# Performance work log

Hardware: AMD Instinct MI355X
Metric: run time of the kernel (lower is better)

## Reference

```python
import jax, jax.numpy as jnp
import numpy as np

B, L, C = 256, 256, 128
HID, H = 128, 4
D = HID // H            # 32
NUM_LAYERS = 2
NEG_SLOPE = 0.2
LN_EPS = 1e-5


def setup_inputs() -> dict:
    key = jax.random.key(0)
    ks = jax.random.split(key, 16)
    E = 4096
    x = jax.random.normal(ks[0], (B, L, C), dtype=jnp.float32)
    edge_index = jax.random.randint(ks[1], (2, E), 0, C, dtype=jnp.int64)
    s_in = 1.0 / np.sqrt(L)
    s_h = 1.0 / np.sqrt(HID)
    return {
        "x": x,
        "edge_index": edge_index,
        "emb_W": jax.random.normal(ks[2], (L, HID), jnp.float32) * s_in,
        "emb_b": jnp.zeros((HID,), jnp.float32),
        "lin_l_W": jax.random.normal(ks[3], (NUM_LAYERS, HID, HID), jnp.float32) * s_h,
        "lin_l_b": jnp.zeros((NUM_LAYERS, HID), jnp.float32),
        "lin_r_W": jax.random.normal(ks[4], (NUM_LAYERS, HID, HID), jnp.float32) * s_h,
        "lin_r_b": jnp.zeros((NUM_LAYERS, HID), jnp.float32),
        "att": jax.random.normal(ks[5], (NUM_LAYERS, H, D), jnp.float32) * (1.0 / np.sqrt(D)),
        "gat_bias": jnp.zeros((NUM_LAYERS, HID), jnp.float32),
        "ln_gamma": jnp.ones((NUM_LAYERS, HID), jnp.float32),
        "ln_beta": jnp.zeros((NUM_LAYERS, HID), jnp.float32),
        "proj_W": jax.random.normal(ks[6], (HID, L), jnp.float32) * s_h,
        "proj_b": jnp.zeros((L,), jnp.float32),
    }


def _batch_edges(edge_index):
    # replicate single-graph edges per batch sample with node offsets, then add self loops
    E = edge_index.shape[1]
    off = jnp.repeat(jnp.arange(B, dtype=edge_index.dtype) * C, E)
    src = jnp.tile(edge_index[0], B) + off
    dst = jnp.tile(edge_index[1], B) + off
    loop = jnp.arange(B * C, dtype=edge_index.dtype)
    return jnp.concatenate([src, loop]), jnp.concatenate([dst, loop])


def _layer_norm(x, g, b):
    mu = jnp.mean(x, axis=-1, keepdims=True)
    var = jnp.mean(jnp.square(x - mu), axis=-1, keepdims=True)
    return (x - mu) * jax.lax.rsqrt(var + LN_EPS) * g + b


def _gatv2(x, src, dst, Wl, bl, Wr, br, a, bias):
    N = x.shape[0]
    xl = (x @ Wl + bl).reshape(N, H, D)   # source-side transform
    xr = (x @ Wr + br).reshape(N, H, D)   # target-side transform
    e = jax.nn.leaky_relu(xl[src] + xr[dst], NEG_SLOPE)   # (E', H, D)
    logits = jnp.einsum('ehd,hd->eh', e, a)               # (E', H)
    m = jax.ops.segment_max(logits, dst, num_segments=N)
    p = jnp.exp(logits - m[dst])
    s = jax.ops.segment_sum(p, dst, num_segments=N)
    alpha = p / (s[dst] + 1e-16)
    out = jax.ops.segment_sum(xl[src] * alpha[:, :, None], dst, num_segments=N)
    return out.reshape(N, HID) + bias, alpha


def reference(x, edge_index, emb_W, emb_b, lin_l_W, lin_l_b, lin_r_W, lin_r_b,
              att, gat_bias, ln_gamma, ln_beta, proj_W, proj_b):
    src, dst = _batch_edges(edge_index)
    # (B, L, C) -> nodes are channels: (B*C, L) -> embed to HID
    h = x.transpose(0, 2, 1).reshape(B * C, L) @ emb_W + emb_b
    alpha = None
    for i in range(NUM_LAYERS):
        new_h, alpha = _gatv2(h, src, dst, lin_l_W[i], lin_l_b[i],
                              lin_r_W[i], lin_r_b[i], att[i], gat_bias[i])
        new_h = jax.nn.elu(new_h)
        h = h + new_h
        h = _layer_norm(h, ln_gamma[i], ln_beta[i])
        # dropout: eval mode, identity
    # attention map (to_dense_adj semantics: adj[b, src%C, dst%C] = mean_h(alpha), then transpose)
    b_idx = src // C
    dense = jnp.zeros((B, C, C), x.dtype).at[b_idx, src % C, dst % C].add(alpha.mean(axis=-1))
    attn_map = dense.transpose(0, 2, 1)
    out = (h @ proj_W + proj_b).reshape(B, C, L).transpose(0, 2, 1)  # (B, L, C)
    return out, attn_map
```

## Files before the change

### kernel.cpp

```cpp
#include <hip/hip_runtime.h>
#include <hip/hip_fp16.h>
#include <math.h>

#define BB 256
#define LL 256
#define CC 128
#define HIDD 128
#define HH 4
#define DD 32
#define EE 4096
#define NN (BB*CC)
#define LN_EPS 1e-5f

typedef short bf16x8 __attribute__((ext_vector_type(8)));
typedef _Float16 f16x8 __attribute__((ext_vector_type(8)));
typedef float f32x4 __attribute__((ext_vector_type(4)));

__device__ __forceinline__ float red64(float p) {
    p += __shfl_xor(p, 32);
    p += __shfl_xor(p, 16);
    p += __shfl_xor(p, 8);
    p += __shfl_xor(p, 4);
    p += __shfl_xor(p, 2);
    p += __shfl_xor(p, 1);
    return p;
}
__device__ __forceinline__ unsigned bfr(float f) {
    unsigned x = __float_as_uint(f);
    return (x + 0x7FFFu + ((x >> 16) & 1u)) >> 16;
}
__device__ __forceinline__ unsigned pack2(float a, float b) { return bfr(a) | (bfr(b) << 16); }
__device__ __forceinline__ float b2f(unsigned u) { return __uint_as_float(u << 16); }
__device__ __forceinline__ __half2 u2h(unsigned u) { __half2 r; *(unsigned*)&r = u; return r; }
__device__ __forceinline__ unsigned h2u(__half2 h) { return *(unsigned*)&h; }

__device__ __forceinline__ void stage_bf16_rm(ushort* lds, const ushort* src, int ldm, int t) {
    #pragma unroll
    for (int i = 0; i < 8; ++i) {
        int flat = i*256 + t;
        int r = flat >> 4, c = flat & 15;
        uint4 pk = *(const uint4*)(src + (size_t)r*ldm + c*8);
        *(uint4*)&lds[((r*16) + (c ^ (r & 7)))*8] = pk;
    }
}
__device__ __forceinline__ void mfma_tile_128(const ushort* Als, const ushort* Bls,
                                              f32x4 acc[2][8], int w, int lane) {
    int mr = lane & 15, quad = lane >> 4;
    #pragma unroll
    for (int ks = 0; ks < 4; ++ks) {
        int ca = ks*4 + quad;
        bf16x8 a[2], b[8];
        #pragma unroll
        for (int mf = 0; mf < 2; ++mf) {
            int m = w*32 + mf*16 + mr;
            a[mf] = *(const bf16x8*)&Als[((m*16) + (ca ^ (m & 7)))*8];
        }
        #pragma unroll
        for (int nf = 0; nf < 8; ++nf) {
            int n = nf*16 + mr;
            b[nf] = *(const bf16x8*)&Bls[((n*16) + (ca ^ (n & 7)))*8];
        }
        #pragma unroll
        for (int mf = 0; mf < 2; ++mf)
            #pragma unroll
            for (int nf = 0; nf < 8; ++nf)
                acc[mf][nf] = __builtin_amdgcn_mfma_f32_16x16x32_bf16(a[mf], b[nf], acc[mf][nf], 0, 0, 0);
    }
}
#define ZERO_ACC(acc) { _Pragma("unroll") for (int i_=0;i_<2;++i_) { _Pragma("unroll") for (int j_=0;j_<8;++j_) acc[i_][j_] = (f32x4){0.f,0.f,0.f,0.f}; } }

__global__ __launch_bounds__(256) void prep_weights(const float* __restrict__ emb_W,
                                                    const float* __restrict__ lWl,
                                                    const float* __restrict__ lWr,
                                                    const float* __restrict__ pW,
                                                    ushort* __restrict__ WembT,
                                                    ushort* __restrict__ WlrT,
                                                    ushort* __restrict__ WpT) {
    int gid = blockIdx.x * 256 + threadIdx.x;
    float v[8];
    if (gid < 4096) {
        int f = gid >> 5, ch = gid & 31;
        #pragma unroll
        for (int j = 0; j < 8; ++j) v[j] = emb_W[(size_t)(ch*8 + j)*HIDD + f];
        uint4 pk; pk.x = pack2(v[0],v[1]); pk.y = pack2(v[2],v[3]);
        pk.z = pack2(v[4],v[5]); pk.w = pack2(v[6],v[7]);
        *(uint4*)&WembT[(size_t)f*LL + ch*8] = pk;
    } else if (gid < 12288) {
        int g = gid - 4096;
        int mat = g >> 11, f = (g >> 4) & 127, ch = g & 15;
        const float* src = ((mat & 1) ? lWr : lWl) + (size_t)(mat >> 1)*HIDD*HIDD;
        #pragma unroll
        for (int j = 0; j < 8; ++j) v[j] = src[(size_t)(ch*8 + j)*HIDD + f];
        uint4 pk; pk.x = pack2(v[0],v[1]); pk.y = pack2(v[2],v[3]);
        pk.z = pack2(v[4],v[5]); pk.w = pack2(v[6],v[7]);
        *(uint4*)&WlrT[(size_t)mat*HIDD*HIDD + (size_t)f*HIDD + ch*8] = pk;
    } else {
        int g = gid - 12288;
        int l = g >> 4, ch = g & 15;
        #pragma unroll
        for (int j = 0; j < 8; ++j) v[j] = pW[(size_t)(ch*8 + j)*LL + l];
        uint4 pk; pk.x = pack2(v[0],v[1]); pk.y = pack2(v[2],v[3]);
        pk.z = pack2(v[4],v[5]); pk.w = pack2(v[6],v[7]);
        *(uint4*)&WpT[(size_t)l*HIDD + ch*8] = pk;
    }
}

__global__ __launch_bounds__(256) void build_lnm(const int* __restrict__ edge,
                                                 __half* __restrict__ lnm_ds) {
    __shared__ int cnt[CC*CC];
    int t = threadIdx.x;
    for (int i = t; i < CC*CC; i += 256) cnt[i] = 0;
    __syncthreads();
    for (int j = t; j < EE; j += 256) {
        int s = edge[j], d = edge[EE + j];
        atomicAdd(&cnt[s*CC + d], 1);
    }
    __syncthreads();
    for (int o = t; o < CC*CC; o += 256) {
        int dstc = o >> 7, srcc = o & 127;
        int c = cnt[srcc*CC + dstc] + ((srcc == dstc) ? 1 : 0);
        lnm_ds[o] = __float2half(c > 0 ? logf((float)c) : -30000.f);
    }
}

__global__ __launch_bounds__(256) void embed_mfma(const float* __restrict__ x,
                                                  const ushort* __restrict__ WembT,
                                                  const float* __restrict__ bias,
                                                  ushort* __restrict__ hout) {
    __shared__ __align__(16) ushort Als[128*16*8];
    __shared__ __align__(16) ushort Bls[128*16*8];
    int b = blockIdx.x;
    int t = threadIdx.x, lane = t & 63, w = t >> 6;
    const float* xb = x + (size_t)b * LL * CC;
    f32x4 acc[2][8];
    ZERO_ACC(acc)
    #pragma unroll
    for (int kh = 0; kh < 2; ++kh) {
        if (kh) __syncthreads();
        #pragma unroll
        for (int i = 0; i < 8; ++i) {
            int flat = i*256 + t;
            int r = flat >> 4, cc = flat & 15;
            float v[8];
            #pragma unroll
            for (int j = 0; j < 8; ++j)
                v[j] = xb[(size_t)(kh*128 + cc*8 + j)*CC + r];
            uint4 pk; pk.x = pack2(v[0],v[1]); pk.y = pack2(v[2],v[3]);
            pk.z = pack2(v[4],v[5]); pk.w = pack2(v[6],v[7]);
            *(uint4*)&Als[((r*16) + (cc ^ (r & 7)))*8] = pk;
        }
        stage_bf16_rm(Bls, WembT + kh*128, LL, t);
        __syncthreads();
        mfma_tile_128(Als, Bls, acc, w, lane);
    }
    int mr = lane & 15, quad = lane >> 4;
    #pragma unroll
    for (int nf = 0; nf < 8; ++nf) {
        int f = nf*16 + mr;
        float bv = bias[f];
        #pragma unroll
        for (int mf = 0; mf < 2; ++mf)
            #pragma unroll
            for (int r = 0; r < 4; ++r) {
                int node = w*32 + mf*16 + quad*4 + r;
                hout[((size_t)b*CC + node)*HIDD + f] = (ushort)bfr(acc[mf][nf][r] + bv);
            }
    }
}

__global__ __launch_bounds__(256) void lin_mfma(const ushort* __restrict__ hmat,
                                                const ushort* __restrict__ WlT,
                                                const ushort* __restrict__ WrT,
                                                const float* __restrict__ bl,
                                                const float* __restrict__ br,
                                                __half* __restrict__ xlT,
                                                __half* __restrict__ xrT) {
    __shared__ __align__(16) ushort Als[128*16*8];
    __shared__ __align__(16) ushort Bls[128*16*8];
    int b = blockIdx.x;
    int t = threadIdx.x, lane = t & 63, w = t >> 6;
    int mr = lane & 15, quad = lane >> 4;
    stage_bf16_rm(Als, hmat + (size_t)b*CC*HIDD, HIDD, t);
    #pragma unroll
    for (int lr = 0; lr < 2; ++lr) {
        if (lr) __syncthreads();
        stage_bf16_rm(Bls, lr ? WrT : WlT, HIDD, t);
        __syncthreads();
        f32x4 acc[2][8];
        ZERO_ACC(acc)
        mfma_tile_128(Als, Bls, acc, w, lane);
        const float* bias = lr ? br : bl;
        __half* out = lr ? xrT : xlT;
        #pragma unroll
        for (int nf = 0; nf < 8; ++nf) {
            int f = nf*16 + mr;
            float bv = bias[f];
            int h = f >> 5, d = f & 31;
            #pragma unroll
            for (int mf = 0; mf < 2; ++mf)
                #pragma unroll
                for (int r = 0; r < 4; ++r) {
                    int node = w*32 + mf*16 + quad*4 + r;
                    out[(((size_t)b*HH + h)*CC + node)*DD + d] = __float2half(acc[mf][nf][r] + bv);
                }
        }
    }
}

__global__ __launch_bounds__(256, 4) void gat_logits(const __half* __restrict__ xl_h,
                                                     const __half* __restrict__ xr_h,
                                                     const __half* __restrict__ lnm_ds,
                                                     const float* __restrict__ att,
                                                     __half* __restrict__ Pg) {
    __shared__ __align__(16) __half xl_lds[CC*DD];
    __shared__ float Slq[CC];
    __shared__ float rpart[2][CC];
    __shared__ float spart[2][CC];

    int bh = blockIdx.x;
    int h = bh & 3;
    int t = threadIdx.x;
    int sg = t >> 7, dst = t & 127;

    {
        const uint4* sp = (const uint4*)(xl_h + (size_t)bh * CC * DD);
        uint4* dp = (uint4*)xl_lds;
        dp[t] = sp[t];
        dp[t + 256] = sp[t + 256];
    }
    __half2 qa2[16], xr2[16];
    const float* ag = att + h*DD;
    #pragma unroll
    for (int c = 0; c < 8; ++c) {
        float4 av = *(const float4*)&ag[c*4];
        qa2[2*c+0] = __floats2half2_rn(0.4f*av.x, 0.4f*av.y);
        qa2[2*c+1] = __floats2half2_rn(0.4f*av.z, 0.4f*av.w);
    }
    float Srq = 0.f;
    {
        uint4 X[4];
        const uint4* xp = (const uint4*)(xr_h + ((size_t)bh*CC + dst)*DD);
        #pragma unroll
        for (int c = 0; c < 4; ++c) X[c] = xp[c];
        const __half2* xv = (const __half2*)X;
        #pragma unroll
        for (int i = 0; i < 16; ++i) {
            xr2[i] = xv[i];
            __half2 p = __hmul2(qa2[i], xr2[i]);
            Srq += __low2float(p) + __high2float(p);
        }
    }
    __syncthreads();

    if (t < CC) {
        uint4 R[4];
        const uint4* rp = (const uint4*)&xl_lds[t*DD];
        #pragma unroll
        for (int c = 0; c < 4; ++c) R[c] = rp[c];
        const __half2* rv = (const __half2*)R;
        __half2 s = __floats2half2_rn(0.f, 0.f);
        #pragma unroll
        for (int i = 0; i < 16; ++i) s = __hfma2(qa2[i], rv[i], s);
        Slq[t] = __low2float(s) + __high2float(s);
    }
    __syncthreads();

    const __half* lrow = lnm_ds + (size_t)dst*CC + sg*64;
    float fSrq = 1.5f * Srq;
    __half2 lv2[32];
    float pmax = -3.0e38f;
    #pragma unroll
    for (int jc = 0; jc < 8; ++jc) {
        int chunk = sg*8 + jc;
        uint4 lu = *(const uint4*)&lrow[jc*8];
        const __half* lnmv = (const __half*)&lu;
        float lf[8];
        #pragma unroll
        for (int e = 0; e < 8; ++e) {
            int src = chunk*8 + e;
            uint4 R[4];
            const uint4* rp = (const uint4*)&xl_lds[src*DD];
            #pragma unroll
            for (int c = 0; c < 4; ++c) R[c] = rp[c];
            const __half2* xv = (const __half2*)R;
            __half2 a0 = __floats2half2_rn(0.f,0.f), a1 = a0, a2 = a0, a3 = a0;
            #pragma unroll
            for (int q = 0; q < 4; ++q) {
                a0 = __hfma2(qa2[4*q+0], __habs2(__hadd2(xv[4*q+0], xr2[4*q+0])), a0);
                a1 = __hfma2(qa2[4*q+1], __habs2(__hadd2(xv[4*q+1], xr2[4*q+1])), a1);
                a2 = __hfma2(qa2[4*q+2], __habs2(__hadd2(xv[4*q+2], xr2[4*q+2])), a2);
                a3 = __hfma2(qa2[4*q+3], __habs2(__hadd2(xv[4*q+3], xr2[4*q+3])), a3);
            }
            __half2 ts = __hadd2(__hadd2(a0, a1), __hadd2(a2, a3));
            float T = __low2float(ts) + __high2float(ts);
            float l = fmaf(1.5f, Slq[src], fSrq + T) + __half2float(lnmv[e]);
            pmax = fmaxf(pmax, l);
            lf[e] = l;
        }
        lv2[jc*4+0] = __floats2half2_rn(lf[0], lf[1]);
        lv2[jc*4+1] = __floats2half2_rn(lf[2], lf[3]);
        lv2[jc*4+2] = __floats2half2_rn(lf[4], lf[5]);
        lv2[jc*4+3] = __floats2half2_rn(lf[6], lf[7]);
    }

    rpart[sg][dst] = pmax;
    __syncthreads();
    float m = fmaxf(rpart[0][dst], rpart[1][dst]);
    float ssum = 0.f;
    #pragma unroll
    for (int i = 0; i < 32; ++i) {
        float e0 = __expf(__low2float(lv2[i]) - m);
        float e1 = __expf(__high2float(lv2[i]) - m);
        ssum += e0 + e1;
        lv2[i] = __floats2half2_rn(e0, e1);
    }
    spart[sg][dst] = ssum;
    __syncthreads();
    float is = 1.f / (spart[0][dst] + spart[1][dst] + 1e-16f);

    __half* pgr = Pg + (size_t)bh*CC*CC + (size_t)dst*CC + sg*64;
    #pragma unroll
    for (int jc = 0; jc < 8; ++jc) {
        __align__(16) __half ov[8];
        #pragma unroll
        for (int i = 0; i < 4; ++i) {
            __half2 v = lv2[jc*4+i];
            ov[2*i+0] = __float2half(__low2float(v) * is);
            ov[2*i+1] = __float2half(__high2float(v) * is);
        }
        *(uint4*)&pgr[jc*8] = *(uint4*)ov;
    }
}

__global__ __launch_bounds__(256) void gat_pv(const __half* __restrict__ Pg,
                                              const __half* __restrict__ xl_h,
                                              __half* __restrict__ xagg) {
    __shared__ __align__(16) __half xl_lds[CC*DD];
    __shared__ __align__(16) __half xlT_swz[DD*16*8];
    int bh = blockIdx.x, h = bh & 3, b = bh >> 2;
    int t = threadIdx.x, lane = t & 63, w = t >> 6;
    {
        const uint4* sp = (const uint4*)(xl_h + (size_t)bh * CC * DD);
        uint4* dp = (uint4*)xl_lds;
        dp[t] = sp[t];
        dp[t + 256] = sp[t + 256];
    }
    __syncthreads();
    for (int i = t; i < 512; i += 256) {
        int f = i >> 4, c = i & 15;
        __align__(16) __half v[8];
        #pragma unroll
        for (int e = 0; e < 8; ++e) v[e] = xl_lds[(c*8 + e)*DD + f];
        *(uint4*)&xlT_swz[((f*16) + (c ^ (f & 7)))*8] = *(uint4*)v;
    }
    __syncthreads();

    int mr = lane & 15, quad = lane >> 4;
    const __half* pb = Pg + (size_t)bh * CC * CC;
    f16x8 a[2][4];
    #pragma unroll
    for (int mf = 0; mf < 2; ++mf) {
        int dr = w*32 + mf*16 + mr;
        #pragma unroll
        for (int ks = 0; ks < 4; ++ks)
            a[mf][ks] = *(const f16x8*)&pb[(size_t)dr*CC + ks*32 + quad*8];
    }
    f32x4 acc[2][2];
    #pragma unroll
    for (int i = 0; i < 2; ++i)
        #pragma unroll
        for (int j = 0; j < 2; ++j) acc[i][j] = (f32x4){0.f,0.f,0.f,0.f};
    #pragma unroll
    for (int ks = 0; ks < 4; ++ks) {
        int ca = ks*4 + quad;
        f16x8 bfrag[2];
        #pragma unroll
        for (int nf = 0; nf < 2; ++nf) {
            int nn = nf*16 + mr;
            bfrag[nf] = *(const f16x8*)&xlT_swz[((nn*16) + (ca ^ (nn & 7)))*8];
        }
        #pragma unroll
        for (int mf = 0; mf < 2; ++mf)
            #pragma unroll
            for (int nf = 0; nf < 2; ++nf)
                acc[mf][nf] = __builtin_amdgcn_mfma_f32_16x16x32_f16(a[mf][ks], bfrag[nf], acc[mf][nf], 0, 0, 0);
    }
    #pragma unroll
    for (int mf = 0; mf < 2; ++mf)
        #pragma unroll
        for (int r = 0; r < 4; ++r) {
            int drow = w*32 + mf*16 + quad*4 + r;
            #pragma unroll
            for (int nf = 0; nf < 2; ++nf) {
                int f = nf*16 + mr;
                xagg[(((size_t)b*CC + drow)*HH + h)*DD + f] = __float2half(acc[mf][nf][r]);
            }
        }
}

__global__ __launch_bounds__(256) void gat_epilogue(const __half* __restrict__ xagg,
                                                    const float* __restrict__ gbias,
                                                    const float* __restrict__ ln_g,
                                                    const float* __restrict__ ln_b,
                                                    const __half* __restrict__ Pws,
                                                    ushort* __restrict__ hmat,
                                                    float* __restrict__ attn_out) {
    __shared__ float wred[4], wred2[4];
    int t = threadIdx.x;
    int nl = t >> 7, f = t & 127;
    int node = blockIdx.x*2 + nl;
    int b = node >> 7, dstc = node & 127;

    float o = __half2float(xagg[(size_t)node*HIDD + f]) + gbias[f];
    o = o > 0.f ? o : (__expf(o) - 1.f);
    float hv = b2f((unsigned)hmat[(size_t)node*HIDD + f]) + o;

    float sum = red64(hv);
    if ((t & 63) == 0) wred[t >> 6] = sum;
    __syncthreads();
    float mean = (wred[nl*2] + wred[nl*2+1]) * 0.0078125f;
    float d = hv - mean;
    float q = red64(d * d);
    if ((t & 63) == 0) wred2[t >> 6] = q;
    __syncthreads();
    float var = (wred2[nl*2] + wred2[nl*2+1]) * 0.0078125f;
    hmat[(size_t)node*HIDD + f] = (ushort)bfr(d * rsqrtf(var + LN_EPS) * ln_g[f] + ln_b[f]);

    if (attn_out) {
        float a = 0.f;
        #pragma unroll
        for (int hh = 0; hh < HH; ++hh)
            a += __half2float(Pws[(((size_t)(b*HH + hh)*CC) + dstc)*CC + f]);
        attn_out[(size_t)node*CC + f] = 0.25f * a;
    }
}

__global__ __launch_bounds__(256) void proj_mfma(const ushort* __restrict__ hmat,
                                                 const ushort* __restrict__ WpT,
                                                 const float* __restrict__ bias,
                                                 float* __restrict__ out) {
    __shared__ __align__(16) ushort Als[128*16*8];
    __shared__ __align__(16) ushort Bls[128*16*8];
    int l0 = blockIdx.x * 128;
    int b  = blockIdx.y;
    int t = threadIdx.x, lane = t & 63, w = t >> 6;
    f32x4 acc[2][8];
    ZERO_ACC(acc)
    stage_bf16_rm(Als, WpT + (size_t)l0*HIDD, HIDD, t);
    stage_bf16_rm(Bls, hmat + (size_t)b*CC*HIDD, HIDD, t);
    __syncthreads();
    mfma_tile_128(Als, Bls, acc, w, lane);
    int mr = lane & 15, quad = lane >> 4;
    #pragma unroll
    for (int nf = 0; nf < 8; ++nf) {
        int c = nf*16 + mr;
        #pragma unroll
        for (int mf = 0; mf < 2; ++mf)
            #pragma unroll
            for (int r = 0; r < 4; ++r) {
                int l = l0 + w*32 + mf*16 + quad*4 + r;
                out[((size_t)b*LL + l)*CC + c] = acc[mf][nf][r] + bias[l];
            }
    }
}

extern "C" void kernel_launch(void* const* d_in, const int* in_sizes, int n_in,
                              void* d_out, int out_size, void* d_ws, size_t ws_size,
                              hipStream_t stream) {
    const float* x        = (const float*)d_in[0];
    const int*   edge     = (const int*)d_in[1];
    const float* emb_W    = (const float*)d_in[2];
    const float* emb_b    = (const float*)d_in[3];
    const float* lin_l_W  = (const float*)d_in[4];
    const float* lin_l_b  = (const float*)d_in[5];
    const float* lin_r_W  = (const float*)d_in[6];
    const float* lin_r_b  = (const float*)d_in[7];
    const float* att      = (const float*)d_in[8];
    const float* gat_bias = (const float*)d_in[9];
    const float* ln_g     = (const float*)d_in[10];
    const float* ln_b     = (const float*)d_in[11];
    const float* proj_W   = (const float*)d_in[12];
    const float* proj_b   = (const float*)d_in[13];

    ushort* h     = (ushort*)d_ws;
    __half* xl_h  = (__half*)(h + (size_t)NN * HIDD);
    __half* xr_h  = xl_h + (size_t)NN * HIDD;
    __half* xagg  = xr_h + (size_t)NN * HIDD;
    __half* Pg    = xagg + (size_t)NN * HIDD;
    __half* lnm_ds = Pg + (size_t)BB * HH * CC * CC;
    ushort* WembT = (ushort*)(lnm_ds + (size_t)CC * CC);
    ushort* WlrT  = WembT + (size_t)CC*LL;
    ushort* WpT   = WlrT + (size_t)4*HIDD*HIDD;

    float* out0 = (float*)d_out;
    float* attn = out0 + (size_t)BB * LL * CC;

    build_lnm<<<1, 256, 0, stream>>>(edge, lnm_ds);
    prep_weights<<<64, 256, 0, stream>>>(emb_W, lin_l_W, lin_r_W, proj_W, WembT, WlrT, WpT);
    embed_mfma<<<BB, 256, 0, stream>>>(x, WembT, emb_b, h);
    for (int layer = 0; layer < 2; ++layer) {
        lin_mfma<<<BB, 256, 0, stream>>>(h,
            WlrT + (size_t)(layer*2 + 0)*HIDD*HIDD,
            WlrT + (size_t)(layer*2 + 1)*HIDD*HIDD,
            lin_l_b + layer*HIDD, lin_r_b + layer*HIDD,
            xl_h, xr_h);
        gat_logits<<<BB*HH, 256, 0, stream>>>(xl_h, xr_h, lnm_ds,
            att + layer*HIDD, Pg);
        gat_pv<<<BB*HH, 256, 0, stream>>>(Pg, xl_h, xagg);
        gat_epilogue<<<NN/2, 256, 0, stream>>>(xagg,
            gat_bias + layer*HIDD, ln_g + layer*HIDD, ln_b + layer*HIDD,
            (layer == 1) ? Pg : nullptr, h, (layer == 1) ? attn : nullptr);
    }
    proj_mfma<<<dim3(2, BB), 256, 0, stream>>>(h, WpT, proj_b, out0);
}
```

Before: 305.9 us.

## Fuse GAT logits/softmax with P·V MFMA and split destinations across blocks

Merges the attention-logit/softmax kernel and the P·xl aggregation kernel into one kernel. The normalized probabilities are kept in LDS in MFMA fragment layout instead of being written to and reread from global memory, and the global P buffer is written only for the last layer, where the attention map needs it. Each block now handles 64 destination nodes with 4 source groups instead of 128 destinations with 2 groups, doubling the grid, and LDS loads of xl rows are double-buffered in registers. The cost is more LDS per block, duplicated xl staging and transposition in both halves, and a fragment-ordered P layout that the epilogue must index to match.

Measured after the change: 296.7 us. 3.0% less time.

```diff
diff --git a/kernel.cpp b/kernel.cpp
--- a/kernel.cpp
+++ b/kernel.cpp
@@ -31,8 +31,6 @@
 }
 __device__ __forceinline__ unsigned pack2(float a, float b) { return bfr(a) | (bfr(b) << 16); }
 __device__ __forceinline__ float b2f(unsigned u) { return __uint_as_float(u << 16); }
-__device__ __forceinline__ __half2 u2h(unsigned u) { __half2 r; *(unsigned*)&r = u; return r; }
-__device__ __forceinline__ unsigned h2u(__half2 h) { return *(unsigned*)&h; }
 
 __device__ __forceinline__ void stage_bf16_rm(ushort* lds, const ushort* src, int ldm, int t) {
     #pragma unroll
@@ -207,20 +205,30 @@
     }
 }
 
-__global__ __launch_bounds__(256, 4) void gat_logits(const __half* __restrict__ xl_h,
-                                                     const __half* __restrict__ xr_h,
-                                                     const __half* __restrict__ lnm_ds,
-                                                     const float* __restrict__ att,
-                                                     __half* __restrict__ Pg) {
+#define LOADC(Rdst, jcv) { _Pragma("unroll") for (int u_ = 0; u_ < 4; ++u_) { \
+    const uint4* rp_ = (const uint4*)&xl_lds[(sg*32 + (jcv)*4 + u_)*DD]; \
+    Rdst[u_][0]=rp_[0]; Rdst[u_][1]=rp_[1]; Rdst[u_][2]=rp_[2]; Rdst[u_][3]=rp_[3]; } }
+
+__global__ __launch_bounds__(256, 4) void gat_fused(const __half* __restrict__ xl_h,
+                                                    const __half* __restrict__ xr_h,
+                                                    const __half* __restrict__ lnm_ds,
+                                                    const float* __restrict__ att,
+                                                    __half* __restrict__ xagg,
+                                                    __half* __restrict__ Pg) {
     __shared__ __align__(16) __half xl_lds[CC*DD];
+    __shared__ __align__(16) __half xlT_swz[DD*16*8];
+    __shared__ __align__(16) __half Pfrag[4*4*64*8];
     __shared__ float Slq[CC];
-    __shared__ float rpart[2][CC];
-    __shared__ float spart[2][CC];
-
-    int bh = blockIdx.x;
-    int h = bh & 3;
+    __shared__ float rpart[4][64];
+    __shared__ float spart[4][64];
+
+    int blk = blockIdx.x;
+    int bh = blk >> 1, dhalf = blk & 1;
+    int h = bh & 3, b = bh >> 2;
     int t = threadIdx.x;
-    int sg = t >> 7, dst = t & 127;
+    int sg = t >> 6, dl = t & 63;
+    int dst = dhalf*64 + dl;
+    int lane = t & 63, w = t >> 6;
 
     {
         const uint4* sp = (const uint4*)(xl_h + (size_t)bh * CC * DD);
@@ -228,6 +236,14 @@
         dp[t] = sp[t];
         dp[t + 256] = sp[t + 256];
     }
+    __align__(16) __half lnm_l[32];
+    {
+        const __half* lrow = lnm_ds + (size_t)dst*CC + sg*32;
+        *(uint4*)&lnm_l[0]  = *(const uint4*)&lrow[0];
+        *(uint4*)&lnm_l[8]  = *(const uint4*)&lrow[8];
+        *(uint4*)&lnm_l[16] = *(const uint4*)&lrow[16];
+        *(uint4*)&lnm_l[24] = *(const uint4*)&lrow[24];
+    }
     __half2 qa2[16], xr2[16];
     const float* ag = att + h*DD;
     #pragma unroll
@@ -261,28 +277,33 @@
         __half2 s = __floats2half2_rn(0.f, 0.f);
         #pragma unroll
         for (int i = 0; i < 16; ++i) s = __hfma2(qa2[i], rv[i], s);
-        Slq[t] = __low2float(s) + __high2float(s);
-    }
-    __syncthreads();
-
-    const __half* lrow = lnm_ds + (size_t)dst*CC + sg*64;
+        Slq[t] = 1.5f * (__low2float(s) + __high2float(s));
+    }
+    for (int i = t; i < 512; i += 256) {
+        int f = i >> 4, c = i & 15;
+        __align__(16) __half v[8];
+        #pragma unroll
+        for (int e = 0; e < 8; ++e) v[e] = xl_lds[(c*8 + e)*DD + f];
+        *(uint4*)&xlT_swz[((f*16) + (c ^ (f & 7)))*8] = *(uint4*)v;
+    }
+    __syncthreads();
+
     float fSrq = 1.5f * Srq;
-    __half2 lv2[32];
-    float pmax = -3.0e38f;
+    __half2 lv2[16];
+    float pm0 = -3.0e38f, pm1 = pm0, pm2 = pm0, pm3 = pm0;
+    uint4 Ra[4][4], Rb[4][4];
+    LOADC(Ra, 0)
+    float lfbuf = 0.f;
     #pragma unroll
     for (int jc = 0; jc < 8; ++jc) {
-        int chunk = sg*8 + jc;
-        uint4 lu = *(const uint4*)&lrow[jc*8];
-        const __half* lnmv = (const __half*)&lu;
-        float lf[8];
-        #pragma unroll
-        for (int e = 0; e < 8; ++e) {
-            int src = chunk*8 + e;
-            uint4 R[4];
-            const uint4* rp = (const uint4*)&xl_lds[src*DD];
-            #pragma unroll
-            for (int c = 0; c < 4; ++c) R[c] = rp[c];
-            const __half2* xv = (const __half2*)R;
+        uint4 (*Rc)[4] = (jc & 1) ? Rb : Ra;
+        uint4 (*Rn)[4] = (jc & 1) ? Ra : Rb;
+        if (jc < 7) LOADC(Rn, jc + 1)
+        #pragma unroll
+        for (int u = 0; u < 4; ++u) {
+            int j = jc*4 + u;
+            int src = sg*32 + j;
+            const __half2* xv = (const __half2*)(Rc[u]);
             __half2 a0 = __floats2half2_rn(0.f,0.f), a1 = a0, a2 = a0, a3 = a0;
             #pragma unroll
             for (int q = 0; q < 4; ++q) {
@@ -293,109 +314,82 @@
             }
             __half2 ts = __hadd2(__hadd2(a0, a1), __hadd2(a2, a3));
             float T = __low2float(ts) + __high2float(ts);
-            float l = fmaf(1.5f, Slq[src], fSrq + T) + __half2float(lnmv[e]);
-            pmax = fmaxf(pmax, l);
-            lf[e] = l;
-        }
-        lv2[jc*4+0] = __floats2half2_rn(lf[0], lf[1]);
-        lv2[jc*4+1] = __floats2half2_rn(lf[2], lf[3]);
-        lv2[jc*4+2] = __floats2half2_rn(lf[4], lf[5]);
-        lv2[jc*4+3] = __floats2half2_rn(lf[6], lf[7]);
-    }
-
-    rpart[sg][dst] = pmax;
-    __syncthreads();
-    float m = fmaxf(rpart[0][dst], rpart[1][dst]);
-    float ssum = 0.f;
-    #pragma unroll
-    for (int i = 0; i < 32; ++i) {
+            float l = (fSrq + T) + Slq[src] + __half2float(lnm_l[j]);
+            if (u == 0)      pm0 = fmaxf(pm0, l);
+            else if (u == 1) pm1 = fmaxf(pm1, l);
+            else if (u == 2) pm2 = fmaxf(pm2, l);
+            else             pm3 = fmaxf(pm3, l);
+            if ((j & 1) == 0) lfbuf = l;
+            else              lv2[j >> 1] = __floats2half2_rn(lfbuf, l);
+        }
+    }
+
+    rpart[sg][dl] = fmaxf(fmaxf(pm0, pm1), fmaxf(pm2, pm3));
+    __syncthreads();
+    float m = fmaxf(fmaxf(rpart[0][dl], rpart[1][dl]),
+                    fmaxf(rpart[2][dl], rpart[3][dl]));
+    float s0 = 0.f, s1 = 0.f, s2 = 0.f, s3 = 0.f;
+    #pragma unroll
+    for (int i = 0; i < 16; ++i) {
         float e0 = __expf(__low2float(lv2[i]) - m);
         float e1 = __expf(__high2float(lv2[i]) - m);
-        ssum += e0 + e1;
+        if ((i & 3) == 0)      s0 += e0 + e1;
+        else if ((i & 3) == 1) s1 += e0 + e1;
+        else if ((i & 3) == 2) s2 += e0 + e1;
+        else                   s3 += e0 + e1;
         lv2[i] = __floats2half2_rn(e0, e1);
     }
-    spart[sg][dst] = ssum;
-    __syncthreads();
-    float is = 1.f / (spart[0][dst] + spart[1][dst] + 1e-16f);
-
-    __half* pgr = Pg + (size_t)bh*CC*CC + (size_t)dst*CC + sg*64;
-    #pragma unroll
-    for (int jc = 0; jc < 8; ++jc) {
-        __align__(16) __half ov[8];
-        #pragma unroll
-        for (int i = 0; i < 4; ++i) {
-            __half2 v = lv2[jc*4+i];
-            ov[2*i+0] = __float2half(__low2float(v) * is);
-            ov[2*i+1] = __float2half(__high2float(v) * is);
-        }
-        *(uint4*)&pgr[jc*8] = *(uint4*)ov;
-    }
-}
-
-__global__ __launch_bounds__(256) void gat_pv(const __half* __restrict__ Pg,
-                                              const __half* __restrict__ xl_h,
-                                              __half* __restrict__ xagg) {
-    __shared__ __align__(16) __half xl_lds[CC*DD];
-    __shared__ __align__(16) __half xlT_swz[DD*16*8];
-    int bh = blockIdx.x, h = bh & 3, b = bh >> 2;
-    int t = threadIdx.x, lane = t & 63, w = t >> 6;
+    spart[sg][dl] = (s0 + s1) + (s2 + s3);
+    __syncthreads();
+    float is = 1.f / (((spart[0][dl] + spart[1][dl]) +
+                       (spart[2][dl] + spart[3][dl])) + 1e-16f);
+
     {
-        const uint4* sp = (const uint4*)(xl_h + (size_t)bh * CC * DD);
-        uint4* dp = (uint4*)xl_lds;
-        dp[t] = sp[t];
-        dp[t + 256] = sp[t + 256];
-    }
-    __syncthreads();
-    for (int i = t; i < 512; i += 256) {
-        int f = i >> 4, c = i & 15;
-        __align__(16) __half v[8];
-        #pragma unroll
-        for (int e = 0; e < 8; ++e) v[e] = xl_lds[(c*8 + e)*DD + f];
-        *(uint4*)&xlT_swz[((f*16) + (c ^ (f & 7)))*8] = *(uint4*)v;
-    }
-    __syncthreads();
-
-    int mr = lane & 15, quad = lane >> 4;
-    const __half* pb = Pg + (size_t)bh * CC * CC;
-    f16x8 a[2][4];
-    #pragma unroll
-    for (int mf = 0; mf < 2; ++mf) {
-        int dr = w*32 + mf*16 + mr;
-        #pragma unroll
-        for (int ks = 0; ks < 4; ++ks)
-            a[mf][ks] = *(const f16x8*)&pb[(size_t)dr*CC + ks*32 + quad*8];
-    }
-    f32x4 acc[2][2];
-    #pragma unroll
-    for (int i = 0; i < 2; ++i)
-        #pragma unroll
-        for (int j = 0; j < 2; ++j) acc[i][j] = (f32x4){0.f,0.f,0.f,0.f};
+        __half* pf = &Pfrag[(((dl >> 4)*4 + sg)*64 + (dl & 15))*8];
+        __half* pgr = Pg ? Pg + (size_t)bh*CC*CC +
+                           ((((size_t)(dst >> 4)*4 + sg)*64 + (dst & 15))*8) : nullptr;
+        #pragma unroll
+        for (int q = 0; q < 4; ++q) {
+            __align__(16) __half ov[8];
+            #pragma unroll
+            for (int i = 0; i < 4; ++i) {
+                __half2 v = lv2[q*4 + i];
+                ov[2*i+0] = __float2half(__low2float(v) * is);
+                ov[2*i+1] = __float2half(__high2float(v) * is);
+            }
+            *(uint4*)&pf[q*128] = *(uint4*)ov;
+            if (pgr) *(uint4*)&pgr[q*128] = *(uint4*)ov;
+        }
+    }
+    __syncthreads();
+
+    int quad = lane >> 4, mr = lane & 15;
+    f16x8 a[4];
+    #pragma unroll
+    for (int ks = 0; ks < 4; ++ks)
+        a[ks] = *(const f16x8*)&Pfrag[((w*4 + ks)*64 + lane)*8];
+    f32x4 acc[2];
+    acc[0] = (f32x4){0.f,0.f,0.f,0.f};
+    acc[1] = (f32x4){0.f,0.f,0.f,0.f};
     #pragma unroll
     for (int ks = 0; ks < 4; ++ks) {
         int ca = ks*4 + quad;
-        f16x8 bfrag[2];
         #pragma unroll
         for (int nf = 0; nf < 2; ++nf) {
-            int nn = nf*16 + mr;
-            bfrag[nf] = *(const f16x8*)&xlT_swz[((nn*16) + (ca ^ (nn & 7)))*8];
-        }
-        #pragma unroll
-        for (int mf = 0; mf < 2; ++mf)
-            #pragma unroll
-            for (int nf = 0; nf < 2; ++nf)
-                acc[mf][nf] = __builtin_amdgcn_mfma_f32_16x16x32_f16(a[mf][ks], bfrag[nf], acc[mf][nf], 0, 0, 0);
-    }
-    #pragma unroll
-    for (int mf = 0; mf < 2; ++mf)
+            int n = nf*16 + mr;
+            f16x8 bf = *(const f16x8*)&xlT_swz[((n*16) + (ca ^ (n & 7)))*8];
+            acc[nf] = __builtin_amdgcn_mfma_f32_16x16x32_f16(a[ks], bf, acc[nf], 0, 0, 0);
+        }
+    }
+    #pragma unroll
+    for (int nf = 0; nf < 2; ++nf) {
+        int f = nf*16 + mr;
         #pragma unroll
         for (int r = 0; r < 4; ++r) {
-            int drow = w*32 + mf*16 + quad*4 + r;
-            #pragma unroll
-            for (int nf = 0; nf < 2; ++nf) {
-                int f = nf*16 + mr;
-                xagg[(((size_t)b*CC + drow)*HH + h)*DD + f] = __float2half(acc[mf][nf][r]);
-            }
-        }
+            int node = dhalf*64 + w*16 + quad*4 + r;
+            xagg[(((size_t)b*CC + node)*HH + h)*DD + f] = __float2half(acc[nf][r]);
+        }
+    }
 }
 
 __global__ __launch_bounds__(256) void gat_epilogue(const __half* __restrict__ xagg,
@@ -427,10 +421,12 @@
     hmat[(size_t)node*HIDD + f] = (ushort)bfr(d * rsqrtf(var + LN_EPS) * ln_g[f] + ln_b[f]);
 
     if (attn_out) {
+        int ks = f >> 5, qq = (f >> 3) & 3, e = f & 7;
+        size_t off = ((size_t)((dstc >> 4)*4 + ks)*64 + qq*16 + (dstc & 15))*8 + e;
         float a = 0.f;
         #pragma unroll
         for (int hh = 0; hh < HH; ++hh)
-            a += __half2float(Pws[(((size_t)(b*HH + hh)*CC) + dstc)*CC + f]);
+            a += __half2float(Pws[(size_t)(b*HH + hh)*CC*CC + off]);
         attn_out[(size_t)node*CC + f] = 0.25f * a;
     }
 }
@@ -504,9 +500,8 @@
             WlrT + (size_t)(layer*2 + 1)*HIDD*HIDD,
             lin_l_b + layer*HIDD, lin_r_b + layer*HIDD,
             xl_h, xr_h);
-        gat_logits<<<BB*HH, 256, 0, stream>>>(xl_h, xr_h, lnm_ds,
-            att + layer*HIDD, Pg);
-        gat_pv<<<BB*HH, 256, 0, stream>>>(Pg, xl_h, xagg);
+        gat_fused<<<BB*HH*2, 256, 0, stream>>>(xl_h, xr_h, lnm_ds,
+            att + layer*HIDD, xagg, (layer == 1) ? Pg : nullptr);
         gat_epilogue<<<NN/2, 256, 0, stream>>>(xagg,
             gat_bias + layer*HIDD, ln_g + layer*HIDD, ln_b + layer*HIDD,
             (layer == 1) ? Pg : nullptr, h, (layer == 1) ? attn : nullptr);
```

## Fuse GAT logits/softmax with PV MFMA, restructure embed loads and edge-count prep

Applied to the files above, without the earlier changes.

Merges the logits/softmax kernel and the attention-value MFMA kernel into one per-(batch,head) kernel. P is written in an MFMA-fragment-swizzled layout and read back within the same block, and the epilogue's attention-map read is remapped to match. Each thread now handles two destination rows over a quarter of the sources, which shares the xl LDS loads across two rows. The edge multiplicity is applied as a multiplier after exp instead of adding a log term. Edge counting is folded into prep_weights as an extra block, and the embed staging reads x with coalesced float4 loads plus a rotated LDS scatter. Together these drop one launch per layer and one global re-read of the xl tile per layer, at the cost of more registers and extra syncs in the fused kernel.

Measured after the change: 317.8 us. 1.04x slower.

```diff
diff --git a/kernel.cpp b/kernel.cpp
--- a/kernel.cpp
+++ b/kernel.cpp
@@ -31,8 +31,6 @@
 }
 __device__ __forceinline__ unsigned pack2(float a, float b) { return bfr(a) | (bfr(b) << 16); }
 __device__ __forceinline__ float b2f(unsigned u) { return __uint_as_float(u << 16); }
-__device__ __forceinline__ __half2 u2h(unsigned u) { __half2 r; *(unsigned*)&r = u; return r; }
-__device__ __forceinline__ unsigned h2u(__half2 h) { return *(unsigned*)&h; }
 
 __device__ __forceinline__ void stage_bf16_rm(ushort* lds, const ushort* src, int ldm, int t) {
     #pragma unroll
@@ -73,10 +71,29 @@
                                                     const float* __restrict__ lWl,
                                                     const float* __restrict__ lWr,
                                                     const float* __restrict__ pW,
+                                                    const int* __restrict__ edge,
                                                     ushort* __restrict__ WembT,
                                                     ushort* __restrict__ WlrT,
-                                                    ushort* __restrict__ WpT) {
-    int gid = blockIdx.x * 256 + threadIdx.x;
+                                                    ushort* __restrict__ WpT,
+                                                    __half* __restrict__ mult_ds) {
+    __shared__ int cnt[CC*CC];
+    int t = threadIdx.x;
+    if (blockIdx.x == 64) {
+        for (int i = t; i < CC*CC; i += 256) cnt[i] = 0;
+        __syncthreads();
+        for (int j = t; j < EE; j += 256) {
+            int s = edge[j], d = edge[EE + j];
+            atomicAdd(&cnt[s*CC + d], 1);
+        }
+        __syncthreads();
+        for (int o = t; o < CC*CC; o += 256) {
+            int dstc = o >> 7, srcc = o & 127;
+            int c = cnt[srcc*CC + dstc] + ((srcc == dstc) ? 1 : 0);
+            mult_ds[o] = __float2half((float)c);
+        }
+        return;
+    }
+    int gid = blockIdx.x * 256 + t;
     float v[8];
     if (gid < 4096) {
         int f = gid >> 5, ch = gid & 31;
@@ -105,24 +122,6 @@
     }
 }
 
-__global__ __launch_bounds__(256) void build_lnm(const int* __restrict__ edge,
-                                                 __half* __restrict__ lnm_ds) {
-    __shared__ int cnt[CC*CC];
-    int t = threadIdx.x;
-    for (int i = t; i < CC*CC; i += 256) cnt[i] = 0;
-    __syncthreads();
-    for (int j = t; j < EE; j += 256) {
-        int s = edge[j], d = edge[EE + j];
-        atomicAdd(&cnt[s*CC + d], 1);
-    }
-    __syncthreads();
-    for (int o = t; o < CC*CC; o += 256) {
-        int dstc = o >> 7, srcc = o & 127;
-        int c = cnt[srcc*CC + dstc] + ((srcc == dstc) ? 1 : 0);
-        lnm_ds[o] = __float2half(c > 0 ? logf((float)c) : -30000.f);
-    }
-}
-
 __global__ __launch_bounds__(256) void embed_mfma(const float* __restrict__ x,
                                                   const ushort* __restrict__ WembT,
                                                   const float* __restrict__ bias,
@@ -131,23 +130,27 @@
     __shared__ __align__(16) ushort Bls[128*16*8];
     int b = blockIdx.x;
     int t = threadIdx.x, lane = t & 63, w = t >> 6;
-    const float* xb = x + (size_t)b * LL * CC;
     f32x4 acc[2][8];
     ZERO_ACC(acc)
     #pragma unroll
     for (int kh = 0; kh < 2; ++kh) {
         if (kh) __syncthreads();
+        const float4* x4 = (const float4*)(x + (size_t)b*LL*CC + (size_t)kh*128*CC);
+        int rot = (t >> 3) & 3;
         #pragma unroll
         for (int i = 0; i < 8; ++i) {
             int flat = i*256 + t;
-            int r = flat >> 4, cc = flat & 15;
-            float v[8];
-            #pragma unroll
-            for (int j = 0; j < 8; ++j)
-                v[j] = xb[(size_t)(kh*128 + cc*8 + j)*CC + r];
-            uint4 pk; pk.x = pack2(v[0],v[1]); pk.y = pack2(v[2],v[3]);
-            pk.z = pack2(v[4],v[5]); pk.w = pack2(v[6],v[7]);
-            *(uint4*)&Als[((r*16) + (cc ^ (r & 7)))*8] = pk;
+            int lp = flat >> 5, c4 = flat & 31;
+            float4 v0 = x4[(size_t)(2*lp)*32 + c4];
+            float4 v1 = x4[(size_t)(2*lp + 1)*32 + c4];
+            int lc = lp >> 2, lh = lp & 3;
+            #pragma unroll
+            for (int j0 = 0; j0 < 4; ++j0) {
+                int j = (j0 + rot) & 3;
+                int c = c4*4 + j;
+                unsigned pk = pack2(((const float*)&v0)[j], ((const float*)&v1)[j]);
+                *(unsigned*)&Als[((c*16) + (lc ^ (c & 7)))*8 + lh*2] = pk;
+            }
         }
         stage_bf16_rm(Bls, WembT + kh*128, LL, t);
         __syncthreads();
@@ -207,20 +210,23 @@
     }
 }
 
-__global__ __launch_bounds__(256, 4) void gat_logits(const __half* __restrict__ xl_h,
-                                                     const __half* __restrict__ xr_h,
-                                                     const __half* __restrict__ lnm_ds,
-                                                     const float* __restrict__ att,
-                                                     __half* __restrict__ Pg) {
+__global__ __launch_bounds__(256, 4) void gat_fused(const __half* __restrict__ xl_h,
+                                                    const __half* __restrict__ xr_h,
+                                                    const __half* __restrict__ mult_ds,
+                                                    const float* __restrict__ att,
+                                                    __half* __restrict__ xagg,
+                                                    __half* __restrict__ Pg) {
     __shared__ __align__(16) __half xl_lds[CC*DD];
+    __shared__ __align__(16) __half xlT_swz[DD*16*8];
     __shared__ float Slq[CC];
-    __shared__ float rpart[2][CC];
-    __shared__ float spart[2][CC];
+    __shared__ float rpart[4][CC];
+    __shared__ float spart[4][CC];
 
     int bh = blockIdx.x;
-    int h = bh & 3;
+    int h = bh & 3, b = bh >> 2;
     int t = threadIdx.x;
-    int sg = t >> 7, dst = t & 127;
+    int sg = t >> 6, dl = t & 63;
+    int dstA = dl, dstB = dl + 64;
 
     {
         const uint4* sp = (const uint4*)(xl_h + (size_t)bh * CC * DD);
@@ -228,7 +234,7 @@
         dp[t] = sp[t];
         dp[t + 256] = sp[t + 256];
     }
-    __half2 qa2[16], xr2[16];
+    __half2 qa2[16];
     const float* ag = att + h*DD;
     #pragma unroll
     for (int c = 0; c < 8; ++c) {
@@ -236,19 +242,26 @@
         qa2[2*c+0] = __floats2half2_rn(0.4f*av.x, 0.4f*av.y);
         qa2[2*c+1] = __floats2half2_rn(0.4f*av.z, 0.4f*av.w);
     }
-    float Srq = 0.f;
+    __half2 xrA[16], xrB[16];
+    float fSA, fSB;
     {
-        uint4 X[4];
-        const uint4* xp = (const uint4*)(xr_h + ((size_t)bh*CC + dst)*DD);
-        #pragma unroll
-        for (int c = 0; c < 4; ++c) X[c] = xp[c];
-        const __half2* xv = (const __half2*)X;
+        uint4 XA[4], XB[4];
+        const uint4* pa = (const uint4*)(xr_h + ((size_t)bh*CC + dstA)*DD);
+        const uint4* pb = (const uint4*)(xr_h + ((size_t)bh*CC + dstB)*DD);
+        #pragma unroll
+        for (int c = 0; c < 4; ++c) { XA[c] = pa[c]; XB[c] = pb[c]; }
+        const __half2* va = (const __half2*)XA;
+        const __half2* vb = (const __half2*)XB;
+        float sA = 0.f, sB = 0.f;
         #pragma unroll
         for (int i = 0; i < 16; ++i) {
-            xr2[i] = xv[i];
-            __half2 p = __hmul2(qa2[i], xr2[i]);
-            Srq += __low2float(p) + __high2float(p);
-        }
+            xrA[i] = va[i]; xrB[i] = vb[i];
+            __half2 p = __hmul2(qa2[i], xrA[i]);
+            sA += __low2float(p) + __high2float(p);
+            __half2 q = __hmul2(qa2[i], xrB[i]);
+            sB += __low2float(q) + __high2float(q);
+        }
+        fSA = 1.5f * sA; fSB = 1.5f * sB;
     }
     __syncthreads();
 
@@ -261,91 +274,8 @@
         __half2 s = __floats2half2_rn(0.f, 0.f);
         #pragma unroll
         for (int i = 0; i < 16; ++i) s = __hfma2(qa2[i], rv[i], s);
-        Slq[t] = __low2float(s) + __high2float(s);
-    }
-    __syncthreads();
-
-    const __half* lrow = lnm_ds + (size_t)dst*CC + sg*64;
-    float fSrq = 1.5f * Srq;
-    __half2 lv2[32];
-    float pmax = -3.0e38f;
-    #pragma unroll
-    for (int jc = 0; jc < 8; ++jc) {
-        int chunk = sg*8 + jc;
-        uint4 lu = *(const uint4*)&lrow[jc*8];
-        const __half* lnmv = (const __half*)&lu;
-        float lf[8];
-        #pragma unroll
-        for (int e = 0; e < 8; ++e) {
-            int src = chunk*8 + e;
-            uint4 R[4];
-            const uint4* rp = (const uint4*)&xl_lds[src*DD];
-            #pragma unroll
-            for (int c = 0; c < 4; ++c) R[c] = rp[c];
-            const __half2* xv = (const __half2*)R;
-            __half2 a0 = __floats2half2_rn(0.f,0.f), a1 = a0, a2 = a0, a3 = a0;
-            #pragma unroll
-            for (int q = 0; q < 4; ++q) {
-                a0 = __hfma2(qa2[4*q+0], __habs2(__hadd2(xv[4*q+0], xr2[4*q+0])), a0);
-                a1 = __hfma2(qa2[4*q+1], __habs2(__hadd2(xv[4*q+1], xr2[4*q+1])), a1);
-                a2 = __hfma2(qa2[4*q+2], __habs2(__hadd2(xv[4*q+2], xr2[4*q+2])), a2);
-                a3 = __hfma2(qa2[4*q+3], __habs2(__hadd2(xv[4*q+3], xr2[4*q+3])), a3);
-            }
-            __half2 ts = __hadd2(__hadd2(a0, a1), __hadd2(a2, a3));
-            float T = __low2float(ts) + __high2float(ts);
-            float l = fmaf(1.5f, Slq[src], fSrq + T) + __half2float(lnmv[e]);
-            pmax = fmaxf(pmax, l);
-            lf[e] = l;
-        }
-        lv2[jc*4+0] = __floats2half2_rn(lf[0], lf[1]);
-        lv2[jc*4+1] = __floats2half2_rn(lf[2], lf[3]);
-        lv2[jc*4+2] = __floats2half2_rn(lf[4], lf[5]);
-        lv2[jc*4+3] = __floats2half2_rn(lf[6], lf[7]);
-    }
-
-    rpart[sg][dst] = pmax;
-    __syncthreads();
-    float m = fmaxf(rpart[0][dst], rpart[1][dst]);
-    float ssum = 0.f;
-    #pragma unroll
-    for (int i = 0; i < 32; ++i) {
-        float e0 = __expf(__low2float(lv2[i]) - m);
-        float e1 = __expf(__high2float(lv2[i]) - m);
-        ssum += e0 + e1;
-        lv2[i] = __floats2half2_rn(e0, e1);
-    }
-    spart[sg][dst] = ssum;
-    __syncthreads();
-    float is = 1.f / (spart[0][dst] + spart[1][dst] + 1e-16f);
-
-    __half* pgr = Pg + (size_t)bh*CC*CC + (size_t)dst*CC + sg*64;
-    #pragma unroll
-    for (int jc = 0; jc < 8; ++jc) {
-        __align__(16) __half ov[8];
-        #pragma unroll
-        for (int i = 0; i < 4; ++i) {
-            __half2 v = lv2[jc*4+i];
-            ov[2*i+0] = __float2half(__low2float(v) * is);
-            ov[2*i+1] = __float2half(__high2float(v) * is);
-        }
-        *(uint4*)&pgr[jc*8] = *(uint4*)ov;
-    }
-}
-
-__global__ __launch_bounds__(256) void gat_pv(const __half* __restrict__ Pg,
-                                              const __half* __restrict__ xl_h,
-                                              __half* __restrict__ xagg) {
-    __shared__ __align__(16) __half xl_lds[CC*DD];
-    __shared__ __align__(16) __half xlT_swz[DD*16*8];
-    int bh = blockIdx.x, h = bh & 3, b = bh >> 2;
-    int t = threadIdx.x, lane = t & 63, w = t >> 6;
-    {
-        const uint4* sp = (const uint4*)(xl_h + (size_t)bh * CC * DD);
-        uint4* dp = (uint4*)xl_lds;
-        dp[t] = sp[t];
-        dp[t + 256] = sp[t + 256];
-    }
-    __syncthreads();
+        Slq[t] = 1.5f * (__low2float(s) + __high2float(s));
+    }
     for (int i = t; i < 512; i += 256) {
         int f = i >> 4, c = i & 15;
         __align__(16) __half v[8];
@@ -355,15 +285,114 @@
     }
     __syncthreads();
 
-    int mr = lane & 15, quad = lane >> 4;
-    const __half* pb = Pg + (size_t)bh * CC * CC;
-    f16x8 a[2][4];
+    __half2 lvA[16], lvB[16];
+    float pmA0 = -3.0e38f, pmA1 = pmA0, pmB0 = pmA0, pmB1 = pmA0;
+    float lbufA = 0.f, lbufB = 0.f;
+    #pragma unroll 4
+    for (int j = 0; j < 32; ++j) {
+        int src = sg*32 + j;
+        uint4 R[4];
+        const uint4* rp = (const uint4*)&xl_lds[src*DD];
+        R[0] = rp[0]; R[1] = rp[1]; R[2] = rp[2]; R[3] = rp[3];
+        float sl = Slq[src];
+        const __half2* xv = (const __half2*)R;
+        __half2 a0 = __floats2half2_rn(0.f,0.f), a1 = a0, a2 = a0, a3 = a0;
+        __half2 b0 = a0, b1 = a0, b2 = a0, b3 = a0;
+        #pragma unroll
+        for (int q = 0; q < 4; ++q) {
+            a0 = __hfma2(qa2[4*q+0], __habs2(__hadd2(xv[4*q+0], xrA[4*q+0])), a0);
+            a1 = __hfma2(qa2[4*q+1], __habs2(__hadd2(xv[4*q+1], xrA[4*q+1])), a1);
+            a2 = __hfma2(qa2[4*q+2], __habs2(__hadd2(xv[4*q+2], xrA[4*q+2])), a2);
+            a3 = __hfma2(qa2[4*q+3], __habs2(__hadd2(xv[4*q+3], xrA[4*q+3])), a3);
+            b0 = __hfma2(qa2[4*q+0], __habs2(__hadd2(xv[4*q+0], xrB[4*q+0])), b0);
+            b1 = __hfma2(qa2[4*q+1], __habs2(__hadd2(xv[4*q+1], xrB[4*q+1])), b1);
+            b2 = __hfma2(qa2[4*q+2], __habs2(__hadd2(xv[4*q+2], xrB[4*q+2])), b2);
+            b3 = __hfma2(qa2[4*q+3], __habs2(__hadd2(xv[4*q+3], xrB[4*q+3])), b3);
+        }
+        __half2 tsA = __hadd2(__hadd2(a0, a1), __hadd2(a2, a3));
+        __half2 tsB = __hadd2(__hadd2(b0, b1), __hadd2(b2, b3));
+        float lA = (fSA + sl) + (__low2float(tsA) + __high2float(tsA));
+        float lB = (fSB + sl) + (__low2float(tsB) + __high2float(tsB));
+        if (j & 1) {
+            pmA1 = fmaxf(pmA1, lA); pmB1 = fmaxf(pmB1, lB);
+            lvA[j >> 1] = __floats2half2_rn(lbufA, lA);
+            lvB[j >> 1] = __floats2half2_rn(lbufB, lB);
+        } else {
+            pmA0 = fmaxf(pmA0, lA); pmB0 = fmaxf(pmB0, lB);
+            lbufA = lA; lbufB = lB;
+        }
+    }
+    rpart[sg][dstA] = fmaxf(pmA0, pmA1);
+    rpart[sg][dstB] = fmaxf(pmB0, pmB1);
+    __syncthreads();
+    float mA = fmaxf(fmaxf(rpart[0][dstA], rpart[1][dstA]),
+                     fmaxf(rpart[2][dstA], rpart[3][dstA]));
+    float mB = fmaxf(fmaxf(rpart[0][dstB], rpart[1][dstB]),
+                     fmaxf(rpart[2][dstB], rpart[3][dstB]));
+
+    uint4 MAr[4], MBr[4];
+    {
+        const uint4* ma = (const uint4*)(mult_ds + (size_t)dstA*CC + sg*32);
+        const uint4* mb = (const uint4*)(mult_ds + (size_t)dstB*CC + sg*32);
+        #pragma unroll
+        for (int c = 0; c < 4; ++c) { MAr[c] = ma[c]; MBr[c] = mb[c]; }
+    }
+    const __half* multA = (const __half*)MAr;
+    const __half* multB = (const __half*)MBr;
+
+    float sA0 = 0.f, sA1 = 0.f, sB0 = 0.f, sB1 = 0.f;
+    #pragma unroll
+    for (int i = 0; i < 16; ++i) {
+        float eA0 = __expf(__low2float(lvA[i]) - mA) * __half2float(multA[2*i]);
+        float eA1 = __expf(__high2float(lvA[i]) - mA) * __half2float(multA[2*i+1]);
+        float eB0 = __expf(__low2float(lvB[i]) - mB) * __half2float(multB[2*i]);
+        float eB1 = __expf(__high2float(lvB[i]) - mB) * __half2float(multB[2*i+1]);
+        if (i & 1) { sA1 += eA0 + eA1; sB1 += eB0 + eB1; }
+        else       { sA0 += eA0 + eA1; sB0 += eB0 + eB1; }
+        lvA[i] = __floats2half2_rn(eA0, eA1);
+        lvB[i] = __floats2half2_rn(eB0, eB1);
+    }
+    spart[sg][dstA] = sA0 + sA1;
+    spart[sg][dstB] = sB0 + sB1;
+    __syncthreads();
+    float isA = 1.f / (((spart[0][dstA] + spart[1][dstA]) +
+                        (spart[2][dstA] + spart[3][dstA])) + 1e-16f);
+    float isB = 1.f / (((spart[0][dstB] + spart[1][dstB]) +
+                        (spart[2][dstB] + spart[3][dstB])) + 1e-16f);
+
+    size_t pbase = (size_t)bh * CC * CC;
+    {
+        int mr = dl & 15, dr0 = dl >> 4;
+        __half* pA = Pg + pbase + (((size_t)(dr0*4 + sg))*64)*8;
+        __half* pB = Pg + pbase + (((size_t)((dr0 + 4)*4 + sg))*64)*8;
+        #pragma unroll
+        for (int q = 0; q < 4; ++q) {
+            int slot = mr*4 + (q ^ (mr & 3));
+            __align__(16) __half ovA[8], ovB[8];
+            #pragma unroll
+            for (int i = 0; i < 4; ++i) {
+                __half2 vA = lvA[q*4 + i], vB = lvB[q*4 + i];
+                ovA[2*i+0] = __float2half(__low2float(vA) * isA);
+                ovA[2*i+1] = __float2half(__high2float(vA) * isA);
+                ovB[2*i+0] = __float2half(__low2float(vB) * isB);
+                ovB[2*i+1] = __float2half(__high2float(vB) * isB);
+            }
+            *(uint4*)&pA[slot*8] = *(uint4*)ovA;
+            *(uint4*)&pB[slot*8] = *(uint4*)ovB;
+        }
+    }
+    __syncthreads();
+
+    int quad = dl >> 4, mr = dl & 15;
+    const __half* pb = Pg + pbase;
+    f16x8 afr[2][4];
     #pragma unroll
     for (int mf = 0; mf < 2; ++mf) {
-        int dr = w*32 + mf*16 + mr;
+        int dr0 = sg*2 + mf;
         #pragma unroll
         for (int ks = 0; ks < 4; ++ks)
-            a[mf][ks] = *(const f16x8*)&pb[(size_t)dr*CC + ks*32 + quad*8];
+            afr[mf][ks] = *(const f16x8*)&pb[(((size_t)(dr0*4 + ks))*64 +
+                                             mr*4 + (quad ^ (mr & 3)))*8];
     }
     f32x4 acc[2][2];
     #pragma unroll
@@ -373,27 +402,27 @@
     #pragma unroll
     for (int ks = 0; ks < 4; ++ks) {
         int ca = ks*4 + quad;
-        f16x8 bfrag[2];
+        f16x8 bfr2[2];
         #pragma unroll
         for (int nf = 0; nf < 2; ++nf) {
-            int nn = nf*16 + mr;
-            bfrag[nf] = *(const f16x8*)&xlT_swz[((nn*16) + (ca ^ (nn & 7)))*8];
+            int n = nf*16 + mr;
+            bfr2[nf] = *(const f16x8*)&xlT_swz[((n*16) + (ca ^ (n & 7)))*8];
         }
         #pragma unroll
         for (int mf = 0; mf < 2; ++mf)
             #pragma unroll
             for (int nf = 0; nf < 2; ++nf)
-                acc[mf][nf] = __builtin_amdgcn_mfma_f32_16x16x32_f16(a[mf][ks], bfrag[nf], acc[mf][nf], 0, 0, 0);
+                acc[mf][nf] = __builtin_amdgcn_mfma_f32_16x16x32_f16(afr[mf][ks], bfr2[nf], acc[mf][nf], 0, 0, 0);
     }
     #pragma unroll
     for (int mf = 0; mf < 2; ++mf)
         #pragma unroll
-        for (int r = 0; r < 4; ++r) {
-            int drow = w*32 + mf*16 + quad*4 + r;
-            #pragma unroll
-            for (int nf = 0; nf < 2; ++nf) {
-                int f = nf*16 + mr;
-                xagg[(((size_t)b*CC + drow)*HH + h)*DD + f] = __float2half(acc[mf][nf][r]);
+        for (int nf = 0; nf < 2; ++nf) {
+            int f = nf*16 + mr;
+            #pragma unroll
+            for (int r = 0; r < 4; ++r) {
+                int node = sg*32 + mf*16 + quad*4 + r;
+                xagg[(((size_t)b*CC + node)*HH + h)*DD + f] = __float2half(acc[mf][nf][r]);
             }
         }
 }
@@ -427,10 +456,14 @@
     hmat[(size_t)node*HIDD + f] = (ushort)bfr(d * rsqrtf(var + LN_EPS) * ln_g[f] + ln_b[f]);
 
     if (attn_out) {
+        int ks = f >> 5, qq = (f >> 3) & 3, e = f & 7;
+        int mr = dstc & 15, dr0 = dstc >> 4;
+        int slot = mr*4 + (qq ^ (mr & 3));
+        size_t off = ((size_t)(dr0*4 + ks)*64 + slot)*8 + e;
         float a = 0.f;
         #pragma unroll
         for (int hh = 0; hh < HH; ++hh)
-            a += __half2float(Pws[(((size_t)(b*HH + hh)*CC) + dstc)*CC + f]);
+            a += __half2float(Pws[(size_t)(b*HH + hh)*CC*CC + off]);
         attn_out[(size_t)node*CC + f] = 0.25f * a;
     }
 }
@@ -487,16 +520,16 @@
     __half* xr_h  = xl_h + (size_t)NN * HIDD;
     __half* xagg  = xr_h + (size_t)NN * HIDD;
     __half* Pg    = xagg + (size_t)NN * HIDD;
-    __half* lnm_ds = Pg + (size_t)BB * HH * CC * CC;
-    ushort* WembT = (ushort*)(lnm_ds + (size_t)CC * CC);
+    __half* mult_ds = Pg + (size_t)BB * HH * CC * CC;
+    ushort* WembT = (ushort*)(mult_ds + (size_t)CC * CC);
     ushort* WlrT  = WembT + (size_t)CC*LL;
     ushort* WpT   = WlrT + (size_t)4*HIDD*HIDD;
 
     float* out0 = (float*)d_out;
     float* attn = out0 + (size_t)BB * LL * CC;
 
-    build_lnm<<<1, 256, 0, stream>>>(edge, lnm_ds);
-    prep_weights<<<64, 256, 0, stream>>>(emb_W, lin_l_W, lin_r_W, proj_W, WembT, WlrT, WpT);
+    prep_weights<<<65, 256, 0, stream>>>(emb_W, lin_l_W, lin_r_W, proj_W, edge,
+                                         WembT, WlrT, WpT, mult_ds);
     embed_mfma<<<BB, 256, 0, stream>>>(x, WembT, emb_b, h);
     for (int layer = 0; layer < 2; ++layer) {
         lin_mfma<<<BB, 256, 0, stream>>>(h,
@@ -504,9 +537,8 @@
             WlrT + (size_t)(layer*2 + 1)*HIDD*HIDD,
             lin_l_b + layer*HIDD, lin_r_b + layer*HIDD,
             xl_h, xr_h);
-        gat_logits<<<BB*HH, 256, 0, stream>>>(xl_h, xr_h, lnm_ds,
-            att + layer*HIDD, Pg);
-        gat_pv<<<BB*HH, 256, 0, stream>>>(Pg, xl_h, xagg);
+        gat_fused<<<BB*HH, 256, 0, stream>>>(xl_h, xr_h, mult_ds,
+            att + layer*HIDD, xagg, Pg);
         gat_epilogue<<<NN/2, 256, 0, stream>>>(xagg,
             gat_bias + layer*HIDD, ln_g + layer*HIDD, ln_b + layer*HIDD,
             (layer == 1) ? Pg : nullptr, h, (layer == 1) ? attn : nullptr);
```
